# Optimization experiments

Hardware: AMD Instinct MI355X
Metric: run time of the kernel (lower is better)

The kernel has to match this reference:

```python
import jax, jax.numpy as jnp
import numpy as np

EMBED_DIM = 1024
NUM_HEADS = 16
HEAD_DIM = EMBED_DIM // NUM_HEADS


def setup_inputs() -> dict:
    key = jax.random.key(0)
    kx, kw1, kb1, kw2, kb2 = jax.random.split(key, 5)
    D = EMBED_DIM
    # torch nn.Linear default init: U(-1/sqrt(in), 1/sqrt(in)); use scaled uniform
    lim = 1.0 / np.sqrt(D)
    return {
        "x": jax.random.normal(kx, (2, 2048, D), dtype=jnp.float32),
        "w_qkv": jax.random.uniform(kw1, (D, 3 * D), jnp.float32, -lim, lim),
        "b_qkv": jax.random.uniform(kb1, (3 * D,), jnp.float32, -lim, lim),
        "w_o": jax.random.uniform(kw2, (D, D), jnp.float32, -lim, lim),
        "b_o": jax.random.uniform(kb2, (D,), jnp.float32, -lim, lim),
    }


def reference(x, w_qkv, b_qkv, w_o, b_o):
    B, S, D = x.shape
    H, hd = NUM_HEADS, HEAD_DIM
    qkv = x @ w_qkv + b_qkv                       # [B,S,3D]
    qkv = qkv.reshape(B, S, H, 3, hd)             # per-head [q|k|v] blocks of size hd
    q = qkv[:, :, :, 0].transpose(0, 2, 1, 3)     # [B,H,S,hd]
    k = qkv[:, :, :, 1].transpose(0, 2, 1, 3)
    v = qkv[:, :, :, 2].transpose(0, 2, 1, 3)
    scale = hd ** -0.5
    scores = jnp.einsum('bhqd,bhkd->bhqk', q, k) * scale
    attn = jax.nn.softmax(scores, axis=-1)
    out = jnp.einsum('bhqk,bhkd->bhqd', attn, v)  # [B,H,S,hd]
    out = out.transpose(0, 2, 1, 3).reshape(B, S, D)
    return out @ w_o + b_o
```

## Files before the change

kernel.cpp:

```cpp
#include <hip/hip_runtime.h>

typedef __attribute__((ext_vector_type(8))) _Float16 half8;
typedef __attribute__((ext_vector_type(4))) _Float16 half4;
typedef __attribute__((ext_vector_type(4))) float f32x4;
typedef __attribute__((ext_vector_type(16))) float f32x16;
typedef __attribute__((ext_vector_type(4))) int i32x4;

typedef __attribute__((address_space(1))) void* gptr_t;
typedef __attribute__((address_space(3))) void* lptr_t;
#define GLL16(g, l) __builtin_amdgcn_global_load_lds((gptr_t)(g), (lptr_t)(l), 16, 0, 0)

__device__ __forceinline__ float fast_exp2(float x) {
  float r;
  asm volatile("v_exp_f32 %0, %1" : "=v"(r) : "v"(x));
  return r;
}


__global__ void cvt_x_kernel(const float* __restrict__ x, _Float16* __restrict__ xh) {
  size_t i = (size_t)blockIdx.x * blockDim.x + threadIdx.x;
  float4 v = *reinterpret_cast<const float4*>(x + i * 4);
  half4 o = { (_Float16)v.x, (_Float16)v.y, (_Float16)v.z, (_Float16)v.w };
  *reinterpret_cast<half4*>(xh + i * 4) = o;
}

__global__ void transpose_cvt_kernel(const float* __restrict__ w, _Float16* __restrict__ wt, int N) {
  __shared__ _Float16 lds[64][72];
  const int t = threadIdx.x;
  const int n0 = blockIdx.x * 64, k0 = blockIdx.y * 64;
#pragma unroll
  for (int rep = 0; rep < 4; ++rep) {
    int k = rep * 16 + (t >> 4);
    int nc = (t & 15) * 4;
    float4 v = *reinterpret_cast<const float4*>(&w[(size_t)(k0 + k) * N + n0 + nc]);
    lds[nc + 0][k] = (_Float16)v.x;
    lds[nc + 1][k] = (_Float16)v.y;
    lds[nc + 2][k] = (_Float16)v.z;
    lds[nc + 3][k] = (_Float16)v.w;
  }
  __syncthreads();
#pragma unroll
  for (int rep = 0; rep < 2; ++rep) {
    int ch = rep * 256 + t;
    int n = ch >> 3, kc = ch & 7;
    half8 o = *reinterpret_cast<const half8*>(&lds[n][kc * 8]);
    *reinterpret_cast<half8*>(&wt[(size_t)(n0 + n) * 1024 + k0 + kc * 8]) = o;
  }
}


__global__ __launch_bounds__(256, 2)
void gemm_qkv(const _Float16* __restrict__ A, const _Float16* __restrict__ Bt,
              const float* __restrict__ bias,
              _Float16* __restrict__ qh, _Float16* __restrict__ kh,
              _Float16* __restrict__ vT) {
  __shared__ __align__(16) _Float16 Ah[128 * 64];
  __shared__ __align__(16) _Float16 Bh[128 * 64];
  const int t = threadIdx.x;
  const int w = t >> 6, ln = t & 63, G = ln >> 4, c = ln & 15;
  const int m0 = blockIdx.y * 128, n0 = blockIdx.x * 128;
  const int wr = w >> 1, wc = w & 1;
  f32x4 acc[4][4] = {};
  for (int kt = 0; kt < 1024; kt += 64) {
#pragma unroll
    for (int i = 0; i < 4; ++i) {
      int ch = i * 256 + t;
      int row = ch >> 3, kc = ch & 7;
      int kk = kt + ((kc ^ (row & 7)) << 3);
      int ldsbase = (i * 256 + w * 64) * 8;
      GLL16(A + (size_t)(m0 + row) * 1024 + kk, Ah + ldsbase);
      GLL16(Bt + (size_t)(n0 + row) * 1024 + kk, Bh + ldsbase);
    }
    __syncthreads();
    half8 aF[2][4], bF[2][4];
#pragma unroll
    for (int ks = 0; ks < 2; ++ks)
#pragma unroll
      for (int i = 0; i < 4; ++i) {
        int ra = wr * 64 + i * 16 + c;
        aF[ks][i] = *reinterpret_cast<const half8*>(&Ah[ra * 64 + (((ks * 4 + G) ^ (ra & 7)) << 3)]);
        int rb = wc * 64 + i * 16 + c;
        bF[ks][i] = *reinterpret_cast<const half8*>(&Bh[rb * 64 + (((ks * 4 + G) ^ (rb & 7)) << 3)]);
      }
#pragma unroll
    for (int ks = 0; ks < 2; ++ks)
#pragma unroll
      for (int mi = 0; mi < 4; ++mi)
#pragma unroll
        for (int ni = 0; ni < 4; ++ni)
          acc[mi][ni] = __builtin_amdgcn_mfma_f32_16x16x32_f16(aF[ks][mi], bF[ks][ni], acc[mi][ni], 0, 0, 0);
    __syncthreads();
  }
  const int mbase = m0 + wr * 64, nbase = n0 + wc * 64;
  const int Gp = ((G & 1) << 1) | (G >> 1);
#pragma unroll
  for (int ni = 0; ni < 4; ++ni) {
    int n = nbase + ni * 16 + c;
    float bv = bias[n];
    int h = n / 192;
    int rem = n - h * 192;
    int tt = rem >> 6, d = rem & 63;
#pragma unroll
    for (int mi = 0; mi < 4; ++mi) {
      if (tt == 2) {
        int mb = mbase + mi * 16;
        int bb = mb >> 11, s0 = mb & 2047;
        size_t bh = (size_t)(bb * 16 + h);
        half4 o = { (_Float16)(acc[mi][ni][0] + bv), (_Float16)(acc[mi][ni][1] + bv),
                    (_Float16)(acc[mi][ni][2] + bv), (_Float16)(acc[mi][ni][3] + bv) };
        *reinterpret_cast<half4*>(&vT[(bh * 64 + d) * 2048 + s0 + 4 * Gp]) = o;
      } else {
#pragma unroll
        for (int r = 0; r < 4; ++r) {
          int m = mbase + mi * 16 + 4 * G + r;
          int bb = m >> 11, s = m & 2047;
          float val = acc[mi][ni][r] + bv;
          size_t bh = (size_t)(bb * 16 + h);
          if (tt == 0) qh[(bh * 2048 + s) * 64 + d] = (_Float16)(val * (0.125f * 1.44269504089f));
          else         kh[(bh * 2048 + s) * 64 + d] = (_Float16)val;
        }
      }
    }
  }
}


__global__ __launch_bounds__(256, 2)
void gemm_o(const _Float16* __restrict__ A, const _Float16* __restrict__ Bt,
            const float* __restrict__ bias, float* __restrict__ outf) {
  __shared__ __align__(16) _Float16 Ah[128 * 64];
  __shared__ __align__(16) _Float16 Bh[64 * 64];
  const int t = threadIdx.x;
  const int w = t >> 6, ln = t & 63, G = ln >> 4, c = ln & 15;
  const int m0 = blockIdx.y * 128, n0 = blockIdx.x * 64;
  const int wr = w >> 1, wc = w & 1;
  f32x4 acc[4][2] = {};
  for (int kt = 0; kt < 1024; kt += 64) {
#pragma unroll
    for (int i = 0; i < 4; ++i) {
      int ch = i * 256 + t;
      int row = ch >> 3, kc = ch & 7;
      int kk = kt + ((kc ^ (row & 7)) << 3);
      GLL16(A + (size_t)(m0 + row) * 1024 + kk, Ah + (i * 256 + w * 64) * 8);
    }
#pragma unroll
    for (int i = 0; i < 2; ++i) {
      int ch = i * 256 + t;
      int row = ch >> 3, kc = ch & 7;
      int kk = kt + ((kc ^ (row & 7)) << 3);
      GLL16(Bt + (size_t)(n0 + row) * 1024 + kk, Bh + (i * 256 + w * 64) * 8);
    }
    __syncthreads();
    half8 aF[2][4], bF[2][2];
#pragma unroll
    for (int ks = 0; ks < 2; ++ks) {
#pragma unroll
      for (int i = 0; i < 4; ++i) {
        int ra = wr * 64 + i * 16 + c;
        aF[ks][i] = *reinterpret_cast<const half8*>(&Ah[ra * 64 + (((ks * 4 + G) ^ (ra & 7)) << 3)]);
      }
#pragma unroll
      for (int i = 0; i < 2; ++i) {
        int rb = wc * 32 + i * 16 + c;
        bF[ks][i] = *reinterpret_cast<const half8*>(&Bh[rb * 64 + (((ks * 4 + G) ^ (rb & 7)) << 3)]);
      }
    }
#pragma unroll
    for (int ks = 0; ks < 2; ++ks)
#pragma unroll
      for (int mi = 0; mi < 4; ++mi)
#pragma unroll
        for (int ni = 0; ni < 2; ++ni)
          acc[mi][ni] = __builtin_amdgcn_mfma_f32_16x16x32_f16(aF[ks][mi], bF[ks][ni], acc[mi][ni], 0, 0, 0);
    __syncthreads();
  }
  const int mbase = m0 + wr * 64, nbase = n0 + wc * 32;
#pragma unroll
  for (int ni = 0; ni < 2; ++ni) {
    int n = nbase + ni * 16 + c;
    float bv = bias[n];
#pragma unroll
    for (int mi = 0; mi < 4; ++mi)
#pragma unroll
      for (int r = 0; r < 4; ++r) {
        int m = mbase + mi * 16 + 4 * G + r;
        outf[(size_t)m * 1024 + n] = acc[mi][ni][r] + bv;
      }
  }
}


__global__ __launch_bounds__(256, 2)
void attn_kernel(const _Float16* __restrict__ qh, const _Float16* __restrict__ kh,
                 const _Float16* __restrict__ vT, _Float16* __restrict__ ao) {
  __shared__ __align__(16) _Float16 Kt[3][64 * 64];
  __shared__ __align__(16) _Float16 Vt[4][64 * 64];
  const int t = threadIdx.x;
  const int w = t >> 6, ln = t & 63, lo = ln & 31, hi = ln >> 5;
  const int bid = blockIdx.x;
  const int xcd = bid & 7, tt = bid >> 3;
  const int bh = xcd * 4 + (tt >> 4);
  const int qb = tt & 15;
  const int q0 = qb * 128 + w * 32;
  const _Float16* qp = qh + (size_t)bh * 2048 * 64;
  const _Float16* kp = kh + (size_t)bh * 2048 * 64;
  const _Float16* vp = vT + (size_t)bh * 64 * 2048;

  half8 qf[4];
#pragma unroll
  for (int sl = 0; sl < 4; ++sl)
    qf[sl] = *reinterpret_cast<const half8*>(qp + (size_t)(q0 + lo) * 64 + sl * 16 + hi * 8);

  f32x16 O0 = {}, O1 = {};
  float plsum = 0.f;
  unsigned pk[4][4];

  auto stage = [&](int kb, int vb, int jt) {
#pragma unroll
    for (int i = 0; i < 2; ++i) {
      int ch = i * 256 + t;
      int row = ch >> 3, cc = ch & 7;
      int sw = ((cc ^ ((row ^ (row >> 3)) & 7)) << 3);
      int ldsbase = (i * 256 + w * 64) * 8;
      GLL16(kp + (size_t)(jt + row) * 64 + sw, &Kt[kb][ldsbase]);
      GLL16(vp + (size_t)row * 2048 + jt + sw, &Vt[vb][ldsbase]);
    }
  };

  auto qkt = [&](int kb, f32x16& s0, f32x16& s1) {
    __builtin_amdgcn_s_setprio(1);
#pragma unroll
    for (int sl = 0; sl < 4; ++sl) {
      const int ch = sl * 2 + hi;
      const int r0 = lo, r1 = 32 + lo;
      half8 k0 = *reinterpret_cast<const half8*>(&Kt[kb][r0 * 64 + ((ch ^ ((r0 ^ (r0 >> 3)) & 7)) << 3)]);
      s0 = __builtin_amdgcn_mfma_f32_32x32x16_f16(k0, qf[sl], s0, 0, 0, 0);
      half8 k1 = *reinterpret_cast<const half8*>(&Kt[kb][r1 * 64 + ((ch ^ ((r1 ^ (r1 >> 3)) & 7)) << 3)]);
      s1 = __builtin_amdgcn_mfma_f32_32x32x16_f16(k1, qf[sl], s1, 0, 0, 0);
    }
    __builtin_amdgcn_s_setprio(0);
  };

  auto pv = [&](int vb) {
    __builtin_amdgcn_s_setprio(1);
#pragma unroll
    for (int kb2 = 0; kb2 < 4; ++kb2) {
      i32x4 pi = { (int)pk[kb2][0], (int)pk[kb2][1], (int)pk[kb2][2], (int)pk[kb2][3] };
      half8 pf = __builtin_bit_cast(half8, pi);
      const int ch = kb2 * 2 + hi;
      const int r0 = lo, r1 = 32 + lo;
      half8 v0 = *reinterpret_cast<const half8*>(&Vt[vb][r0 * 64 + ((ch ^ ((r0 ^ (r0 >> 3)) & 7)) << 3)]);
      O0 = __builtin_amdgcn_mfma_f32_32x32x16_f16(v0, pf, O0, 0, 0, 0);
      half8 v1 = *reinterpret_cast<const half8*>(&Vt[vb][r1 * 64 + ((ch ^ ((r1 ^ (r1 >> 3)) & 7)) << 3)]);
      O1 = __builtin_amdgcn_mfma_f32_32x32x16_f16(v1, pf, O1, 0, 0, 0);
    }
    __builtin_amdgcn_s_setprio(0);
  };

  auto smpack = [&](f32x16& s0, f32x16& s1) {
#pragma unroll
    for (int i = 0; i < 16; ++i) s0[i] = fast_exp2(s0[i]);
#pragma unroll
    for (int i = 0; i < 16; ++i) s1[i] = fast_exp2(s1[i]);
    float sm[8];
#pragma unroll
    for (int i = 0; i < 8; ++i) sm[i] = (s0[i] + s0[i + 8]) + (s1[i] + s1[i + 8]);
#pragma unroll
    for (int i = 0; i < 4; ++i) sm[i] += sm[i + 4];
    plsum += (sm[0] + sm[1]) + (sm[2] + sm[3]);
#pragma unroll
    for (int kh2 = 0; kh2 < 2; ++kh2)
#pragma unroll
      for (int j = 0; j < 4; ++j) {
        pk[kh2][j]     = __builtin_bit_cast(unsigned, __builtin_amdgcn_cvt_pkrtz(s0[kh2 * 8 + 2 * j], s0[kh2 * 8 + 2 * j + 1]));
        pk[2 + kh2][j] = __builtin_bit_cast(unsigned, __builtin_amdgcn_cvt_pkrtz(s1[kh2 * 8 + 2 * j], s1[kh2 * 8 + 2 * j + 1]));
      }
  };

  stage(0, 0, 0);
  stage(1, 1, 64);
  stage(2, 2, 128);
  asm volatile("s_waitcnt vmcnt(8)" ::: "memory");
  __builtin_amdgcn_s_barrier();
  {
    f32x16 s0 = {}, s1 = {};
    qkt(0, s0, s1);
    smpack(s0, s1);
  }
  asm volatile("s_waitcnt vmcnt(4)" ::: "memory");
  __builtin_amdgcn_s_barrier();

  for (int it = 0; it < 31; ++it) {
    if (it < 29) {
      int T = it + 3;
      stage(T % 3, T & 3, T * 64);
    }
    f32x16 s0 = {}, s1 = {};
    qkt((it + 1) % 3, s0, s1);
    pv(it & 3);
    smpack(s0, s1);
    if (it < 29) asm volatile("s_waitcnt vmcnt(4)" ::: "memory");
    else         asm volatile("s_waitcnt vmcnt(0)" ::: "memory");
    __builtin_amdgcn_s_barrier();
  }
  pv(31 & 3);

  float lsum = plsum + __shfl_xor(plsum, 32);
  float inv = 1.f / lsum;
  const int bb = bh >> 4, hd_i = bh & 15;
  const size_t srow = (size_t)bb * 2048 + q0 + lo;
  _Float16* aob = ao + srow * 1024 + hd_i * 64 + hi * 4;
#pragma unroll
  for (int rq = 0; rq < 4; ++rq) {
    half4 o0 = { (_Float16)(O0[4 * rq] * inv), (_Float16)(O0[4 * rq + 1] * inv),
                 (_Float16)(O0[4 * rq + 2] * inv), (_Float16)(O0[4 * rq + 3] * inv) };
    *reinterpret_cast<half4*>(aob + rq * 8) = o0;
    half4 o1 = { (_Float16)(O1[4 * rq] * inv), (_Float16)(O1[4 * rq + 1] * inv),
                 (_Float16)(O1[4 * rq + 2] * inv), (_Float16)(O1[4 * rq + 3] * inv) };
    *reinterpret_cast<half4*>(aob + 32 + rq * 8) = o1;
  }
}


extern "C" void kernel_launch(void* const* d_in, const int* in_sizes, int n_in,
                              void* d_out, int out_size, void* d_ws, size_t ws_size,
                              hipStream_t stream) {
  const float* x     = (const float*)d_in[0];
  const float* w_qkv = (const float*)d_in[1];
  const float* b_qkv = (const float*)d_in[2];
  const float* w_o   = (const float*)d_in[3];
  const float* b_o   = (const float*)d_in[4];
  float* out = (float*)d_out;
  char* ws = (char*)d_ws;
  _Float16* xh    = (_Float16*)(ws);
  _Float16* wqkvT = (_Float16*)(ws + ((size_t)8  << 20));
  _Float16* woT   = (_Float16*)(ws + ((size_t)14 << 20));
  _Float16* qh    = (_Float16*)(ws + ((size_t)16 << 20));
  _Float16* kh    = (_Float16*)(ws + ((size_t)24 << 20));
  _Float16* vT    = (_Float16*)(ws + ((size_t)32 << 20));
  _Float16* ao    = (_Float16*)(ws + ((size_t)40 << 20));

  cvt_x_kernel<<<4096, 256, 0, stream>>>(x, xh);
  transpose_cvt_kernel<<<dim3(48, 16), 256, 0, stream>>>(w_qkv, wqkvT, 3072);
  transpose_cvt_kernel<<<dim3(16, 16), 256, 0, stream>>>(w_o, woT, 1024);
  gemm_qkv<<<dim3(24, 32), 256, 0, stream>>>(xh, wqkvT, b_qkv, qh, kh, vT);
  attn_kernel<<<512, 256, 0, stream>>>(qh, kh, vT, ao);
  gemm_o<<<dim3(16, 32), 256, 0, stream>>>(ao, woT, b_o, out);
}
```

Measured before the change: 119.6 us.

## Merge prep kernels and software-pipeline softmax ahead of QK^T and PV MFMAs

Folds the x conversion and both weight transpose-convert kernels into one launch, dispatching on block index, to cut two launches. In the attention loop, exp/pack of the previous score tile now runs before the current QK^T and PV MFMAs, which sit inside a single high-priority region. Scores are carried across iterations in S0/S1. Launch bounds drop to one block per SM, which allows more registers but may lower occupancy.

```diff
diff --git a/kernel.cpp b/kernel.cpp
--- a/kernel.cpp
+++ b/kernel.cpp
@@ -17,17 +17,23 @@
 }
 
 
-__global__ void cvt_x_kernel(const float* __restrict__ x, _Float16* __restrict__ xh) {
-  size_t i = (size_t)blockIdx.x * blockDim.x + threadIdx.x;
-  float4 v = *reinterpret_cast<const float4*>(x + i * 4);
-  half4 o = { (_Float16)v.x, (_Float16)v.y, (_Float16)v.z, (_Float16)v.w };
-  *reinterpret_cast<half4*>(xh + i * 4) = o;
-}
-
-__global__ void transpose_cvt_kernel(const float* __restrict__ w, _Float16* __restrict__ wt, int N) {
+__global__ void prep_kernel(const float* __restrict__ x, _Float16* __restrict__ xh,
+                            const float* __restrict__ w_qkv, _Float16* __restrict__ wqkvT,
+                            const float* __restrict__ w_o, _Float16* __restrict__ woT) {
   __shared__ _Float16 lds[64][72];
+  const int bid = blockIdx.x;
   const int t = threadIdx.x;
-  const int n0 = blockIdx.x * 64, k0 = blockIdx.y * 64;
+  if (bid < 4096) {
+    size_t i = (size_t)bid * 256 + t;
+    float4 v = *reinterpret_cast<const float4*>(x + i * 4);
+    half4 o = { (_Float16)v.x, (_Float16)v.y, (_Float16)v.z, (_Float16)v.w };
+    *reinterpret_cast<half4*>(xh + i * 4) = o;
+    return;
+  }
+  const float* w; _Float16* wt; int N, bx, by;
+  if (bid < 4096 + 768) { int b = bid - 4096; w = w_qkv; wt = wqkvT; N = 3072; bx = b % 48; by = b / 48; }
+  else                  { int b = bid - 4864; w = w_o;   wt = woT;   N = 1024; bx = b & 15; by = b >> 4; }
+  const int n0 = bx * 64, k0 = by * 64;
 #pragma unroll
   for (int rep = 0; rep < 4; ++rep) {
     int k = rep * 16 + (t >> 4);
@@ -190,7 +196,7 @@
 }
 
 
-__global__ __launch_bounds__(256, 2)
+__global__ __launch_bounds__(256, 1)
 void attn_kernel(const _Float16* __restrict__ qh, const _Float16* __restrict__ kh,
                  const _Float16* __restrict__ vT, _Float16* __restrict__ ao) {
   __shared__ __align__(16) _Float16 Kt[3][64 * 64];
@@ -212,6 +218,7 @@
     qf[sl] = *reinterpret_cast<const half8*>(qp + (size_t)(q0 + lo) * 64 + sl * 16 + hi * 8);
 
   f32x16 O0 = {}, O1 = {};
+  f32x16 S0, S1;
   float plsum = 0.f;
   unsigned pk[4][4];
 
@@ -227,22 +234,21 @@
     }
   };
 
-  auto qkt = [&](int kb, f32x16& s0, f32x16& s1) {
-    __builtin_amdgcn_s_setprio(1);
+  auto qkt = [&](int kb) {
+    f32x16 a = {}, b = {};
 #pragma unroll
     for (int sl = 0; sl < 4; ++sl) {
       const int ch = sl * 2 + hi;
       const int r0 = lo, r1 = 32 + lo;
       half8 k0 = *reinterpret_cast<const half8*>(&Kt[kb][r0 * 64 + ((ch ^ ((r0 ^ (r0 >> 3)) & 7)) << 3)]);
-      s0 = __builtin_amdgcn_mfma_f32_32x32x16_f16(k0, qf[sl], s0, 0, 0, 0);
+      a = __builtin_amdgcn_mfma_f32_32x32x16_f16(k0, qf[sl], a, 0, 0, 0);
       half8 k1 = *reinterpret_cast<const half8*>(&Kt[kb][r1 * 64 + ((ch ^ ((r1 ^ (r1 >> 3)) & 7)) << 3)]);
-      s1 = __builtin_amdgcn_mfma_f32_32x32x16_f16(k1, qf[sl], s1, 0, 0, 0);
-    }
-    __builtin_amdgcn_s_setprio(0);
+      b = __builtin_amdgcn_mfma_f32_32x32x16_f16(k1, qf[sl], b, 0, 0, 0);
+    }
+    S0 = a; S1 = b;
   };
 
   auto pv = [&](int vb) {
-    __builtin_amdgcn_s_setprio(1);
 #pragma unroll
     for (int kb2 = 0; kb2 < 4; ++kb2) {
       i32x4 pi = { (int)pk[kb2][0], (int)pk[kb2][1], (int)pk[kb2][2], (int)pk[kb2][3] };
@@ -254,17 +260,17 @@
       half8 v1 = *reinterpret_cast<const half8*>(&Vt[vb][r1 * 64 + ((ch ^ ((r1 ^ (r1 >> 3)) & 7)) << 3)]);
       O1 = __builtin_amdgcn_mfma_f32_32x32x16_f16(v1, pf, O1, 0, 0, 0);
     }
-    __builtin_amdgcn_s_setprio(0);
   };
 
-  auto smpack = [&](f32x16& s0, f32x16& s1) {
-#pragma unroll
-    for (int i = 0; i < 16; ++i) s0[i] = fast_exp2(s0[i]);
-#pragma unroll
-    for (int i = 0; i < 16; ++i) s1[i] = fast_exp2(s1[i]);
+  auto smpack = [&]() {
+    float e0[16], e1[16];
+#pragma unroll
+    for (int i = 0; i < 16; ++i) e0[i] = fast_exp2(S0[i]);
+#pragma unroll
+    for (int i = 0; i < 16; ++i) e1[i] = fast_exp2(S1[i]);
     float sm[8];
 #pragma unroll
-    for (int i = 0; i < 8; ++i) sm[i] = (s0[i] + s0[i + 8]) + (s1[i] + s1[i + 8]);
+    for (int i = 0; i < 8; ++i) sm[i] = (e0[i] + e0[i + 8]) + (e1[i] + e1[i + 8]);
 #pragma unroll
     for (int i = 0; i < 4; ++i) sm[i] += sm[i + 4];
     plsum += (sm[0] + sm[1]) + (sm[2] + sm[3]);
@@ -272,8 +278,8 @@
     for (int kh2 = 0; kh2 < 2; ++kh2)
 #pragma unroll
       for (int j = 0; j < 4; ++j) {
-        pk[kh2][j]     = __builtin_bit_cast(unsigned, __builtin_amdgcn_cvt_pkrtz(s0[kh2 * 8 + 2 * j], s0[kh2 * 8 + 2 * j + 1]));
-        pk[2 + kh2][j] = __builtin_bit_cast(unsigned, __builtin_amdgcn_cvt_pkrtz(s1[kh2 * 8 + 2 * j], s1[kh2 * 8 + 2 * j + 1]));
+        pk[kh2][j]     = __builtin_bit_cast(unsigned, __builtin_amdgcn_cvt_pkrtz(e0[kh2 * 8 + 2 * j], e0[kh2 * 8 + 2 * j + 1]));
+        pk[2 + kh2][j] = __builtin_bit_cast(unsigned, __builtin_amdgcn_cvt_pkrtz(e1[kh2 * 8 + 2 * j], e1[kh2 * 8 + 2 * j + 1]));
       }
   };
 
@@ -282,11 +288,7 @@
   stage(2, 2, 128);
   asm volatile("s_waitcnt vmcnt(8)" ::: "memory");
   __builtin_amdgcn_s_barrier();
-  {
-    f32x16 s0 = {}, s1 = {};
-    qkt(0, s0, s1);
-    smpack(s0, s1);
-  }
+  qkt(0);
   asm volatile("s_waitcnt vmcnt(4)" ::: "memory");
   __builtin_amdgcn_s_barrier();
 
@@ -295,14 +297,16 @@
       int T = it + 3;
       stage(T % 3, T & 3, T * 64);
     }
-    f32x16 s0 = {}, s1 = {};
-    qkt((it + 1) % 3, s0, s1);
+    smpack();
+    __builtin_amdgcn_s_setprio(1);
+    qkt((it + 1) % 3);
     pv(it & 3);
-    smpack(s0, s1);
+    __builtin_amdgcn_s_setprio(0);
     if (it < 29) asm volatile("s_waitcnt vmcnt(4)" ::: "memory");
     else         asm volatile("s_waitcnt vmcnt(0)" ::: "memory");
     __builtin_amdgcn_s_barrier();
   }
+  smpack();
   pv(31 & 3);
 
   float lsum = plsum + __shfl_xor(plsum, 32);
@@ -340,9 +344,7 @@
   _Float16* vT    = (_Float16*)(ws + ((size_t)32 << 20));
   _Float16* ao    = (_Float16*)(ws + ((size_t)40 << 20));
 
-  cvt_x_kernel<<<4096, 256, 0, stream>>>(x, xh);
-  transpose_cvt_kernel<<<dim3(48, 16), 256, 0, stream>>>(w_qkv, wqkvT, 3072);
-  transpose_cvt_kernel<<<dim3(16, 16), 256, 0, stream>>>(w_o, woT, 1024);
+  prep_kernel<<<5120, 256, 0, stream>>>(x, xh, w_qkv, wqkvT, w_o, woT);
   gemm_qkv<<<dim3(24, 32), 256, 0, stream>>>(xh, wqkvT, b_qkv, qh, kh, vT);
   attn_kernel<<<512, 256, 0, stream>>>(qh, kh, vT, ao);
   gemm_o<<<dim3(16, 32), 256, 0, stream>>>(ao, woT, b_o, out);
```

New measurement: 114.2 us. 1.05x faster.
